# Performance work log

Hardware: AMD Instinct MI355X
Metric: run time of the kernel (lower is better)

## Reference

```python
import jax, jax.numpy as jnp
import numpy as np

B, T, E, D, A, H, C, K = 32, 1500, 512, 512, 512, 4, 10, 201
SHARPENING = 1.0


def setup_inputs() -> dict:
    key = jax.random.key(0)
    ks = jax.random.split(key, 11)
    def w(k, shape, fan_in):
        return jax.random.normal(k, shape, jnp.float32) / np.sqrt(fan_in).astype(np.float32)
    return {
        "enc_out": jax.random.normal(ks[0], (B, T, E), jnp.float32),
        "x_lens": jax.random.randint(ks[1], (B,), T // 2, T + 1),
        "dec_out": jax.random.normal(ks[2], (B, 1, D), jnp.float32),
        # previous-step attention weights: a valid distribution over T per head
        "aw_step": jax.nn.softmax(jax.random.normal(ks[3], (B, T, H), jnp.float32), axis=1),
        "w_enc": w(ks[4], (H, E, A), E),   # per-head LinearND(enc->att)
        "b_enc": jnp.zeros((H, A), jnp.float32),
        "w_dec": w(ks[5], (H, D, A), D),   # per-head LinearND(dec->att), no bias
        "w_conv": w(ks[6], (H, C, A), C),  # per-head LinearND(conv_ch->att), no bias
        "conv_k": w(ks[7], (H * C, 1, K), K),  # grouped 1D conv kernels (O,I,K), groups=H
        "v": w(ks[8], (H, A), A),          # per-head LinearND(att->1), no bias
        "w_mha": w(ks[9], (H * E, E), H * E),
        "b_mha": jnp.zeros((E,), jnp.float32),
    }


def reference(enc_out, x_lens, dec_out, aw_step, w_enc, b_enc, w_dec, w_conv, conv_k, v, w_mha, b_mha):
    b, t, e = enc_out.shape
    h = aw_step.shape[-1]
    c = w_conv.shape[1]
    k = conv_k.shape[-1]
    # enc_out_a: per-head encoder projection [B,T,H,A]
    enc_a = jnp.einsum('bte,hea->btha', enc_out, w_enc) + b_enc
    # decoder projection, broadcast over time [B,1,H,A]
    dec_a = jnp.einsum('bd,hda->bha', dec_out[:, 0], w_dec)[:, None]
    # location features: grouped 1D conv over previous attention weights
    aw_t = jnp.transpose(aw_step, (0, 2, 1))  # [B,H,T]
    conv = jax.lax.conv_general_dilated(
        aw_t, conv_k, window_strides=(1,), padding=[(k // 2, k // 2)],
        dimension_numbers=('NCH', 'OIH', 'NCH'), feature_group_count=h)  # [B,H*C,T]
    conv = conv.reshape(b, h, c, t).transpose(0, 3, 1, 2)  # [B,T,H,C]
    conv_a = jnp.einsum('bthc,hca->btha', conv, w_conv)
    # additive energy [B,T,H]
    energy = jnp.einsum('btha,ha->bth', jnp.tanh(enc_a + dec_a + conv_a), v)
    # original code multiplies energy by mask (1 valid, -1024 padded) then sharpening
    mask = jnp.where(jnp.arange(t)[None, :] < x_lens[:, None], 1.0, -1024.0).astype(energy.dtype)
    energy = energy * mask[:, :, None] * SHARPENING
    aw = jax.nn.softmax(energy, axis=1)  # softmax over time per head
    # per-head context, concatenated along feature dim -> [B,1,H*E]
    ctx = jnp.einsum('bte,bth->bhe', enc_out, aw).reshape(b, 1, h * e)
    ctx = ctx @ w_mha + b_mha  # [B,1,E]
    return ctx, aw
```

## Files before the change

kernel.cpp:

```cpp
#include <hip/hip_runtime.h>
#include <hip/hip_bf16.h>

#define BB 32
#define TT 1500
#define TP 1536
#define EE 512
#define HH 4
#define AA 512
#define NN 2048
#define CC 10
#define KCONV 201
#define KAUG 576

typedef __attribute__((ext_vector_type(8))) __bf16 bf16x8;
typedef __attribute__((ext_vector_type(4))) float f32x4;

__device__ __forceinline__ unsigned short f2bf(float x) {
    unsigned int u = __float_as_uint(x);
    u = (u + 0x7fffu + ((u >> 16) & 1u)) >> 16;
    return (unsigned short)u;
}
__device__ __forceinline__ float bf2f(unsigned short u) {
    return __uint_as_float(((unsigned int)u) << 16);
}
__device__ __forceinline__ void glds16(const void* g, void* l) {
    __builtin_amdgcn_global_load_lds(
        (const __attribute__((address_space(1))) unsigned int*)g,
        (__attribute__((address_space(3))) unsigned int*)l, 16, 0, 0);
}
__device__ __forceinline__ float tanh_fast(float x) {
    float e = __expf(x * 2.0f);
    return fmaf(-2.0f, __builtin_amdgcn_rcpf(e + 1.0f), 1.0f);
}

#define PREP_DEC0   0
#define PREP_CONV0  1024
#define PREP_WT0    8704
#define PREP_PAD0   13312
#define PREP_ENC0   20404
#define PREP_TOTAL  44404

__global__ __launch_bounds__(256) void k_prep(
    const float* __restrict__ enc, const int* __restrict__ xl,
    const float* __restrict__ dec_out, const float* __restrict__ aw_step,
    const float* __restrict__ w_enc, const float* __restrict__ b_enc,
    const float* __restrict__ w_dec, const float* __restrict__ w_conv,
    const float* __restrict__ conv_k,
    unsigned short* __restrict__ Whi, unsigned short* __restrict__ Wlo,
    unsigned short* __restrict__ Ahi, unsigned short* __restrict__ Alo,
    float* __restrict__ dec_a) {
    __shared__ float sbuf[456 + KCONV];
    const int bid = blockIdx.x;
    const int tid = threadIdx.x;

    if (bid < PREP_CONV0) {
        const int b  = bid >> 5;
        const int n0 = (bid & 31) * 64;
        const int n  = n0 + (tid & 63);
        const int dg = tid >> 6;
        const int h  = n >> 9, a = n & 511;
        const float* dp = dec_out + (size_t)b * 512 + dg * 128;
        const float* wp = w_dec + ((size_t)h * 512 + dg * 128) * 512 + a;
        float acc = 0.f;
#pragma unroll 8
        for (int d = 0; d < 128; ++d) acc += dp[d] * wp[(size_t)d * 512];
        sbuf[tid] = acc;
        __syncthreads();
        if (tid < 64) {
            float tot = sbuf[tid] + sbuf[tid + 64] + sbuf[tid + 128] + sbuf[tid + 192];
            dec_a[(size_t)b * NN + n0 + tid] = b_enc[n0 + tid] + tot;
        }
    } else if (bid < PREP_WT0) {
        int r = bid - PREP_CONV0;
        const int tch = r % 6;
        const int hc  = (r / 6) % 40;
        const int b   = r / 240;
        const int h   = hc / 10;
        const int t0  = tch * 256;
        float* sAw = sbuf;
        float* sK  = sbuf + 456;
        for (int i = tid; i < 456; i += 256) {
            int ts = t0 - 100 + i;
            sAw[i] = (ts >= 0 && ts < TT) ? aw_step[((size_t)b * TT + ts) * HH + h] : 0.f;
        }
        if (tid < KCONV) sK[tid] = conv_k[(size_t)hc * KCONV + tid];
        __syncthreads();
        int t = t0 + tid;
        if (t < TT) {
            float acc = 0.f;
            for (int k = 0; k < KCONV; ++k) acc += sAw[tid + k] * sK[k];
            size_t o = ((size_t)b * TP + t) * KAUG + 512 + hc;
            unsigned short hi = f2bf(acc);
            Ahi[o] = hi; Alo[o] = f2bf(acc - bf2f(hi));
        }
    } else if (bid < PREP_PAD0) {
        int idx = (bid - PREP_WT0) * 256 + tid;
        int n = idx / KAUG, k = idx % KAUG;
        int h = n >> 9, a = n & 511;
        float val = 0.f;
        if (k < 512) {
            val = w_enc[((size_t)h * 512 + k) * 512 + a];
        } else if (k < 552) {
            int j = k - 512; int h2 = j / 10, c = j % 10;
            if (h2 == h) val = w_conv[((size_t)h * 10 + c) * 512 + a];
        }
        unsigned short hi = f2bf(val);
        Whi[idx] = hi;
        Wlo[idx] = f2bf(val - bf2f(hi));
    } else if (bid < PREP_ENC0) {
        int idx = (bid - PREP_PAD0) * 256 + tid;
        const int tot1 = BB * 36 * KAUG;
        const int tot2 = BB * TT * 24;
        size_t o;
        if (idx < tot1) {
            int b = idx / (36 * KAUG); int r2 = idx % (36 * KAUG);
            int t = 1500 + r2 / KAUG;  int k = r2 % KAUG;
            o = ((size_t)b * TP + t) * KAUG + k;
        } else if (idx < tot1 + tot2) {
            int j = idx - tot1;
            int b = j / (TT * 24); int r2 = j % (TT * 24);
            int t = r2 / 24;       int k = 552 + r2 % 24;
            o = ((size_t)b * TP + t) * KAUG + k;
        } else return;
        Ahi[o] = 0; Alo[o] = 0;
    } else {
        long idx = (long)(bid - PREP_ENC0) * 256 + tid;
        if (idx >= 6144000L) return;
        long f = idx * 4;
        int b = (int)(f / 768000);
        int r2 = (int)(f % 768000);
        int t = r2 >> 9, e = r2 & 511;
        float4 vv = *reinterpret_cast<const float4*>(enc + f);
        ushort4 h4;
        h4.x = f2bf(vv.x); h4.y = f2bf(vv.y); h4.z = f2bf(vv.z); h4.w = f2bf(vv.w);
        size_t o = ((size_t)b * TP + t) * KAUG + e;
        *reinterpret_cast<ushort4*>(Ahi + o) = h4;
        if (((t & ~127) + 128) > xl[b]) {
            ushort4 l4;
            l4.x = f2bf(vv.x - bf2f(h4.x));
            l4.y = f2bf(vv.y - bf2f(h4.y));
            l4.z = f2bf(vv.z - bf2f(h4.z));
            l4.w = f2bf(vv.w - bf2f(h4.w));
            *reinterpret_cast<ushort4*>(Alo + o) = l4;
        }
    }
}

__global__ __launch_bounds__(256) void k_gemm(
    const unsigned short* __restrict__ Ahi, const unsigned short* __restrict__ Alo,
    const unsigned short* __restrict__ Whi, const unsigned short* __restrict__ Wlo,
    const float* __restrict__ dec_a, const float* __restrict__ vvec,
    const int* __restrict__ xl, float* __restrict__ energy) {
    __shared__ unsigned short lsAhi[128 * 32], lsAlo[128 * 32];
    __shared__ unsigned short lsBhi[128 * 32], lsBlo[128 * 32];
    const int ntile = blockIdx.x, mtile = blockIdx.y, b = blockIdx.z;
    const int tid = threadIdx.x;
    const int lane = tid & 63, wave = tid >> 6;
    const int wm = wave >> 1, wn = wave & 1;
    const int m0 = mtile * 128, n0 = ntile * 128;
    const int xlen = xl[b];

    f32x4 acc[4][4];
#pragma unroll
    for (int i = 0; i < 4; i++)
#pragma unroll
        for (int j = 0; j < 4; j++) acc[i][j] = (f32x4){0.f, 0.f, 0.f, 0.f};

    const int row = tid >> 2;
    const int ko  = (tid & 3) * 8;
    const size_t abase = ((size_t)b * TP + m0 + row) * KAUG + ko;
    const size_t bbase = ((size_t)n0 + row) * KAUG + ko;
    const int l1 = row * 32 + ko;
    const int l2 = l1 + 64 * 32;
    const int ar = wm * 64, br = wn * 64;
    const int fo = (lane & 15) * 32 + (lane >> 4) * 8;

    if (m0 + 128 > xlen) {
        for (int ks = 0; ks < 18; ++ks) {
            const int k0 = ks * 32;
            __syncthreads();
            glds16(Ahi + abase + k0,                     &lsAhi[l1]);
            glds16(Ahi + abase + k0 + (size_t)64 * KAUG, &lsAhi[l2]);
            glds16(Alo + abase + k0,                     &lsAlo[l1]);
            glds16(Alo + abase + k0 + (size_t)64 * KAUG, &lsAlo[l2]);
            glds16(Whi + bbase + k0,                     &lsBhi[l1]);
            glds16(Whi + bbase + k0 + (size_t)64 * KAUG, &lsBhi[l2]);
            glds16(Wlo + bbase + k0,                     &lsBlo[l1]);
            glds16(Wlo + bbase + k0 + (size_t)64 * KAUG, &lsBlo[l2]);
            asm volatile("s_waitcnt vmcnt(0)" ::: "memory");
            __syncthreads();

            bf16x8 ah[4], al[4], bh[4], bl[4];
#pragma unroll
            for (int i = 0; i < 4; i++) {
                ah[i] = *(const bf16x8*)&lsAhi[(ar + i * 16) * 32 + fo];
                al[i] = *(const bf16x8*)&lsAlo[(ar + i * 16) * 32 + fo];
                bh[i] = *(const bf16x8*)&lsBhi[(br + i * 16) * 32 + fo];
                bl[i] = *(const bf16x8*)&lsBlo[(br + i * 16) * 32 + fo];
            }
#pragma unroll
            for (int i = 0; i < 4; i++)
#pragma unroll
                for (int j = 0; j < 4; j++) {
                    acc[i][j] = __builtin_amdgcn_mfma_f32_16x16x32_bf16(ah[i], bh[j], acc[i][j], 0, 0, 0);
                    acc[i][j] = __builtin_amdgcn_mfma_f32_16x16x32_bf16(ah[i], bl[j], acc[i][j], 0, 0, 0);
                    acc[i][j] = __builtin_amdgcn_mfma_f32_16x16x32_bf16(al[i], bh[j], acc[i][j], 0, 0, 0);
                }
        }
    } else {
        for (int ks = 0; ks < 18; ++ks) {
            const int k0 = ks * 32;
            __syncthreads();
            glds16(Ahi + abase + k0,                     &lsAhi[l1]);
            glds16(Ahi + abase + k0 + (size_t)64 * KAUG, &lsAhi[l2]);
            glds16(Whi + bbase + k0,                     &lsBhi[l1]);
            glds16(Whi + bbase + k0 + (size_t)64 * KAUG, &lsBhi[l2]);
            asm volatile("s_waitcnt vmcnt(0)" ::: "memory");
            __syncthreads();

            bf16x8 ah[4], bh[4];
#pragma unroll
            for (int i = 0; i < 4; i++) {
                ah[i] = *(const bf16x8*)&lsAhi[(ar + i * 16) * 32 + fo];
                bh[i] = *(const bf16x8*)&lsBhi[(br + i * 16) * 32 + fo];
            }
#pragma unroll
            for (int i = 0; i < 4; i++)
#pragma unroll
                for (int j = 0; j < 4; j++)
                    acc[i][j] = __builtin_amdgcn_mfma_f32_16x16x32_bf16(ah[i], bh[j], acc[i][j], 0, 0, 0);
        }
    }

    const int h = ntile >> 2;
    const int kg = lane >> 4;
    float dv[4], vv[4];
#pragma unroll
    for (int j = 0; j < 4; j++) {
        int ng = n0 + wn * 64 + j * 16 + (lane & 15);
        dv[j] = dec_a[(size_t)b * NN + ng];
        vv[j] = vvec[ng];
    }
#pragma unroll
    for (int i = 0; i < 4; i++) {
        float part[4] = {0.f, 0.f, 0.f, 0.f};
#pragma unroll
        for (int j = 0; j < 4; j++)
#pragma unroll
            for (int r = 0; r < 4; r++)
                part[r] += tanh_fast(acc[i][j][r] + dv[j]) * vv[j];
#pragma unroll
        for (int r = 0; r < 4; r++) {
            float s = part[r];
            s += __shfl_xor(s, 1, 64);
            s += __shfl_xor(s, 2, 64);
            s += __shfl_xor(s, 4, 64);
            s += __shfl_xor(s, 8, 64);
            if ((lane & 15) == 0) {
                int t = m0 + wm * 64 + i * 16 + kg * 4 + r;
                if (t < TT)
                    atomicAdd(&energy[((size_t)b * HH + h) * TP + t], s);
            }
        }
    }
}

__global__ __launch_bounds__(512) void k_softmax(const float* __restrict__ energy,
                                                 const int* __restrict__ x_lens,
                                                 float* __restrict__ aw) {
    const int b = blockIdx.x >> 2, h = blockIdx.x & 3;
    const int tid = threadIdx.x;
    __shared__ float sE[TT];
    __shared__ float red[512];
    const int xlen = x_lens[b];
    float lmax = -3.4e38f;
    for (int t = tid; t < TT; t += 512) {
        float e = energy[((size_t)b * HH + h) * TP + t];
        float m = (t < xlen) ? e : e * -1024.0f;
        sE[t] = m;
        lmax = fmaxf(lmax, m);
    }
    red[tid] = lmax; __syncthreads();
    for (int s = 256; s > 0; s >>= 1) { if (tid < s) red[tid] = fmaxf(red[tid], red[tid + s]); __syncthreads(); }
    float mx = red[0]; __syncthreads();
    float lsum = 0.f;
    for (int t = tid; t < TT; t += 512) {
        float ex = expf(sE[t] - mx);
        sE[t] = ex; lsum += ex;
    }
    red[tid] = lsum; __syncthreads();
    for (int s = 256; s > 0; s >>= 1) { if (tid < s) red[tid] += red[tid + s]; __syncthreads(); }
    float sum = red[0];
    for (int t = tid; t < TT; t += 512)
        aw[((size_t)b * TT + t) * HH + h] = sE[t] / sum;
}

__global__ __launch_bounds__(512) void k_ctx(const float* __restrict__ enc,
                                             const float* __restrict__ aw,
                                             float* __restrict__ ctx_h) {
    const int chunk = blockIdx.x, b = blockIdx.y;
    const int t0 = chunk * 128;
    const int nt = (TT - t0 < 128) ? (TT - t0) : 128;
    __shared__ float sA[128 * 4];
    const int tid = threadIdx.x;
    for (int i = tid; i < nt * 4; i += 512)
        sA[i] = aw[((size_t)b * TT + t0) * HH + i];
    __syncthreads();
    float a0 = 0.f, a1 = 0.f, a2 = 0.f, a3 = 0.f;
    const float* ep = enc + ((size_t)b * TT + t0) * EE + tid;
    if (nt == 128) {
#pragma unroll 8
        for (int tt = 0; tt < 128; ++tt) {
            float ev = ep[(size_t)tt * EE];
            a0 += sA[tt * 4 + 0] * ev; a1 += sA[tt * 4 + 1] * ev;
            a2 += sA[tt * 4 + 2] * ev; a3 += sA[tt * 4 + 3] * ev;
        }
    } else {
        for (int tt = 0; tt < nt; ++tt) {
            float ev = ep[(size_t)tt * EE];
            a0 += sA[tt * 4 + 0] * ev; a1 += sA[tt * 4 + 1] * ev;
            a2 += sA[tt * 4 + 2] * ev; a3 += sA[tt * 4 + 3] * ev;
        }
    }
    atomicAdd(&ctx_h[((size_t)b * HH + 0) * EE + tid], a0);
    atomicAdd(&ctx_h[((size_t)b * HH + 1) * EE + tid], a1);
    atomicAdd(&ctx_h[((size_t)b * HH + 2) * EE + tid], a2);
    atomicAdd(&ctx_h[((size_t)b * HH + 3) * EE + tid], a3);
}

__global__ __launch_bounds__(256) void k_mha(const float* __restrict__ ctx_h,
                                             const float* __restrict__ w_mha,
                                             const float* __restrict__ b_mha,
                                             float* __restrict__ out) {
    __shared__ float sred[256];
    const int tid = threadIdx.x;
    const int b  = blockIdx.x >> 2;
    const int eo = ((blockIdx.x & 3) << 7) + (tid & 127);
    const int kg = tid >> 7;
    const float* c = ctx_h + (size_t)b * NN + kg * 1024;
    const float* w = w_mha + ((size_t)kg * 1024) * EE + eo;
    float acc = 0.f;
#pragma unroll 8
    for (int k = 0; k < 1024; ++k) acc += c[k] * w[(size_t)k * EE];
    sred[tid] = acc;
    __syncthreads();
    if (tid < 128)
        out[(size_t)b * EE + eo] = b_mha[eo] + sred[tid] + sred[tid + 128];
}

extern "C" void kernel_launch(void* const* d_in, const int* in_sizes, int n_in,
                              void* d_out, int out_size, void* d_ws, size_t ws_size,
                              hipStream_t stream) {
    (void)in_sizes; (void)n_in; (void)out_size;
    const float* enc    = (const float*)d_in[0];
    const int*   xlen   = (const int*)d_in[1];
    const float* dec    = (const float*)d_in[2];
    const float* aw_in  = (const float*)d_in[3];
    const float* w_enc  = (const float*)d_in[4];
    const float* b_enc  = (const float*)d_in[5];
    const float* w_dec  = (const float*)d_in[6];
    const float* w_conv = (const float*)d_in[7];
    const float* convk  = (const float*)d_in[8];
    const float* v      = (const float*)d_in[9];
    const float* w_mha  = (const float*)d_in[10];
    const float* b_mha  = (const float*)d_in[11];
    float* out = (float*)d_out;

    char* ws = (char*)d_ws;
    unsigned short* Whi = (unsigned short*)ws;
    unsigned short* Wlo = Whi + (size_t)NN * KAUG;
    unsigned short* Ahi = (unsigned short*)(ws + 4718592);
    unsigned short* Alo = Ahi + (size_t)BB * TP * KAUG;
    float* dec_a  = (float*)(ws + 117964800);
    float* energy = (float*)(ws + 118226944);
    float* ctx_h  = (float*)(ws + 119013376);
    (void)ws_size;

    hipMemsetAsync(energy, 0, 786432 + 262144, stream);

    k_prep<<<dim3(PREP_TOTAL), 256, 0, stream>>>(enc, xlen, dec, aw_in, w_enc, b_enc,
                                                 w_dec, w_conv, convk,
                                                 Whi, Wlo, Ahi, Alo, dec_a);
    k_gemm<<<dim3(16, 12, BB), 256, 0, stream>>>(Ahi, Alo, Whi, Wlo, dec_a, v, xlen, energy);
    k_softmax<<<dim3(BB * HH), 512, 0, stream>>>(energy, xlen, out + 16384);
    k_ctx <<<dim3(12, BB), 512, 0, stream>>>(enc, out + 16384, ctx_h);
    k_mha <<<dim3(128), 256, 0, stream>>>(ctx_h, w_mha, b_mha, out);
}
```

Before: 597.1 us.

## Fuse enc bf16 split into GEMM, transpose weights via LDS, trim softmax/ctx

The GEMM now reads fp32 encoder rows straight from global memory and converts them to bf16 hi/lo in registers before storing to LDS. This drops the large prep pass that materialised a padded bf16 copy of enc_out. Conv features go to a small separate buffer, the weight transpose goes through a padded LDS tile, and GEMM blocks are remapped so neighbouring tiles land on the same XCD. Softmax moves to 1024 threads with fast exp and a reciprocal, and ctx blocks skip chunks whose weights are all zero. The trade-off is register-path conversion and a software-prefetched A load instead of async global-to-LDS copies.

```diff
diff --git a/kernel.cpp b/kernel.cpp
--- a/kernel.cpp
+++ b/kernel.cpp
@@ -32,24 +32,31 @@
     float e = __expf(x * 2.0f);
     return fmaf(-2.0f, __builtin_amdgcn_rcpf(e + 1.0f), 1.0f);
 }
+__device__ __forceinline__ unsigned int pkbf(float x, float y) {
+    float2 f{x, y};
+    __hip_bfloat162 h2 = __float22bfloat162_rn(f);
+    return *reinterpret_cast<unsigned int*>(&h2);
+}
+__device__ __forceinline__ void split2(float x, float y, unsigned int& h, unsigned int& l) {
+    unsigned short hx = f2bf(x), hy = f2bf(y);
+    h = ((unsigned int)hy << 16) | hx;
+    l = pkbf(x - bf2f(hx), y - bf2f(hy));
+}
 
 #define PREP_DEC0   0
 #define PREP_CONV0  1024
 #define PREP_WT0    8704
-#define PREP_PAD0   13312
-#define PREP_ENC0   20404
-#define PREP_TOTAL  44404
+#define PREP_TOTAL  8992
 
 __global__ __launch_bounds__(256) void k_prep(
-    const float* __restrict__ enc, const int* __restrict__ xl,
     const float* __restrict__ dec_out, const float* __restrict__ aw_step,
     const float* __restrict__ w_enc, const float* __restrict__ b_enc,
     const float* __restrict__ w_dec, const float* __restrict__ w_conv,
     const float* __restrict__ conv_k,
     unsigned short* __restrict__ Whi, unsigned short* __restrict__ Wlo,
-    unsigned short* __restrict__ Ahi, unsigned short* __restrict__ Alo,
+    unsigned short* __restrict__ Chi, unsigned short* __restrict__ Clo,
     float* __restrict__ dec_a) {
-    __shared__ float sbuf[456 + KCONV];
+    __shared__ float sh[64 * 65];
     const int bid = blockIdx.x;
     const int tid = threadIdx.x;
 
@@ -64,10 +71,10 @@
         float acc = 0.f;
 #pragma unroll 8
         for (int d = 0; d < 128; ++d) acc += dp[d] * wp[(size_t)d * 512];
-        sbuf[tid] = acc;
+        sh[tid] = acc;
         __syncthreads();
         if (tid < 64) {
-            float tot = sbuf[tid] + sbuf[tid + 64] + sbuf[tid + 128] + sbuf[tid + 192];
+            float tot = sh[tid] + sh[tid + 64] + sh[tid + 128] + sh[tid + 192];
             dec_a[(size_t)b * NN + n0 + tid] = b_enc[n0 + tid] + tot;
         }
     } else if (bid < PREP_WT0) {
@@ -77,83 +84,77 @@
         const int b   = r / 240;
         const int h   = hc / 10;
         const int t0  = tch * 256;
-        float* sAw = sbuf;
-        float* sK  = sbuf + 456;
+        float* sAw = sh;
         for (int i = tid; i < 456; i += 256) {
             int ts = t0 - 100 + i;
             sAw[i] = (ts >= 0 && ts < TT) ? aw_step[((size_t)b * TT + ts) * HH + h] : 0.f;
         }
-        if (tid < KCONV) sK[tid] = conv_k[(size_t)hc * KCONV + tid];
         __syncthreads();
         int t = t0 + tid;
         if (t < TT) {
+            const float* ck = conv_k + (size_t)hc * KCONV;
             float acc = 0.f;
-            for (int k = 0; k < KCONV; ++k) acc += sAw[tid + k] * sK[k];
-            size_t o = ((size_t)b * TP + t) * KAUG + 512 + hc;
+#pragma unroll 4
+            for (int k = 0; k < KCONV; ++k) acc += sAw[tid + k] * ck[k];
+            size_t o = ((size_t)b * TP + t) * 64 + hc;
             unsigned short hi = f2bf(acc);
-            Ahi[o] = hi; Alo[o] = f2bf(acc - bf2f(hi));
-        }
-    } else if (bid < PREP_PAD0) {
-        int idx = (bid - PREP_WT0) * 256 + tid;
-        int n = idx / KAUG, k = idx % KAUG;
-        int h = n >> 9, a = n & 511;
-        float val = 0.f;
-        if (k < 512) {
-            val = w_enc[((size_t)h * 512 + k) * 512 + a];
-        } else if (k < 552) {
-            int j = k - 512; int h2 = j / 10, c = j % 10;
-            if (h2 == h) val = w_conv[((size_t)h * 10 + c) * 512 + a];
-        }
-        unsigned short hi = f2bf(val);
-        Whi[idx] = hi;
-        Wlo[idx] = f2bf(val - bf2f(hi));
-    } else if (bid < PREP_ENC0) {
-        int idx = (bid - PREP_PAD0) * 256 + tid;
-        const int tot1 = BB * 36 * KAUG;
-        const int tot2 = BB * TT * 24;
-        size_t o;
-        if (idx < tot1) {
-            int b = idx / (36 * KAUG); int r2 = idx % (36 * KAUG);
-            int t = 1500 + r2 / KAUG;  int k = r2 % KAUG;
-            o = ((size_t)b * TP + t) * KAUG + k;
-        } else if (idx < tot1 + tot2) {
-            int j = idx - tot1;
-            int b = j / (TT * 24); int r2 = j % (TT * 24);
-            int t = r2 / 24;       int k = 552 + r2 % 24;
-            o = ((size_t)b * TP + t) * KAUG + k;
-        } else return;
-        Ahi[o] = 0; Alo[o] = 0;
+            Chi[o] = hi; Clo[o] = f2bf(acc - bf2f(hi));
+        }
     } else {
-        long idx = (long)(bid - PREP_ENC0) * 256 + tid;
-        if (idx >= 6144000L) return;
-        long f = idx * 4;
-        int b = (int)(f / 768000);
-        int r2 = (int)(f % 768000);
-        int t = r2 >> 9, e = r2 & 511;
-        float4 vv = *reinterpret_cast<const float4*>(enc + f);
-        ushort4 h4;
-        h4.x = f2bf(vv.x); h4.y = f2bf(vv.y); h4.z = f2bf(vv.z); h4.w = f2bf(vv.w);
-        size_t o = ((size_t)b * TP + t) * KAUG + e;
-        *reinterpret_cast<ushort4*>(Ahi + o) = h4;
-        if (((t & ~127) + 128) > xl[b]) {
-            ushort4 l4;
-            l4.x = f2bf(vv.x - bf2f(h4.x));
-            l4.y = f2bf(vv.y - bf2f(h4.y));
-            l4.z = f2bf(vv.z - bf2f(h4.z));
-            l4.w = f2bf(vv.w - bf2f(h4.w));
-            *reinterpret_cast<ushort4*>(Alo + o) = l4;
+        int r = bid - PREP_WT0;
+        const int h  = r / 72;
+        const int rr = r % 72;
+        const int at = rr / 9;
+        const int kt = rr % 9;
+        const int a0 = at * 64;
+        if (kt < 8) {
+            const int k0 = kt * 64;
+#pragma unroll
+            for (int it = 0; it < 16; ++it) {
+                int kk = it * 4 + (tid >> 6);
+                int aa = tid & 63;
+                sh[kk * 65 + aa] = w_enc[((size_t)h * 512 + k0 + kk) * 512 + a0 + aa];
+            }
+            __syncthreads();
+#pragma unroll
+            for (int it = 0; it < 16; ++it) {
+                int nl = it * 4 + (tid >> 6);
+                int kk = tid & 63;
+                float val = sh[kk * 65 + nl];
+                size_t o = ((size_t)h * 512 + a0 + nl) * KAUG + k0 + kk;
+                unsigned short hi = f2bf(val);
+                Whi[o] = hi; Wlo[o] = f2bf(val - bf2f(hi));
+            }
+        } else {
+#pragma unroll
+            for (int it = 0; it < 16; ++it) {
+                int nl = it * 4 + (tid >> 6);
+                int j  = tid & 63;
+                float val = 0.f;
+                if (j < 40 && (j / 10) == h)
+                    val = w_conv[((size_t)h * 10 + (j % 10)) * 512 + a0 + nl];
+                size_t o = ((size_t)h * 512 + a0 + nl) * KAUG + 512 + j;
+                unsigned short hi = f2bf(val);
+                Whi[o] = hi; Wlo[o] = f2bf(val - bf2f(hi));
+            }
         }
     }
 }
 
 __global__ __launch_bounds__(256) void k_gemm(
-    const unsigned short* __restrict__ Ahi, const unsigned short* __restrict__ Alo,
+    const float* __restrict__ enc,
+    const unsigned short* __restrict__ Chi, const unsigned short* __restrict__ Clo,
     const unsigned short* __restrict__ Whi, const unsigned short* __restrict__ Wlo,
     const float* __restrict__ dec_a, const float* __restrict__ vvec,
     const int* __restrict__ xl, float* __restrict__ energy) {
-    __shared__ unsigned short lsAhi[128 * 32], lsAlo[128 * 32];
-    __shared__ unsigned short lsBhi[128 * 32], lsBlo[128 * 32];
-    const int ntile = blockIdx.x, mtile = blockIdx.y, b = blockIdx.z;
+    __shared__ unsigned short lsAhi[4096], lsAlo[4096];
+    __shared__ unsigned short lsBhi[4096], lsBlo[4096];
+    const int id = blockIdx.x;
+    const int xcd = id & 7;
+    const int wq  = id >> 3;
+    const int ntile = wq & 15;
+    const int mb = xcd * 48 + (wq >> 4);
+    const int b = mb & 31, mtile = mb >> 5;
     const int tid = threadIdx.x;
     const int lane = tid & 63, wave = tid >> 6;
     const int wm = wave >> 1, wn = wave & 1;
@@ -168,25 +169,97 @@
 
     const int row = tid >> 2;
     const int ko  = (tid & 3) * 8;
-    const size_t abase = ((size_t)b * TP + m0 + row) * KAUG + ko;
     const size_t bbase = ((size_t)n0 + row) * KAUG + ko;
-    const int l1 = row * 32 + ko;
-    const int l2 = l1 + 64 * 32;
+    const size_t cbase = ((size_t)b * TP + m0 + row) * 64 + ko;
+    const int l1 = tid * 8;
+    const int l2 = l1 + 2048;
     const int ar = wm * 64, br = wn * 64;
     const int fo = (lane & 15) * 32 + (lane >> 4) * 8;
 
-    if (m0 + 128 > xlen) {
+    const float* ap0 = enc + ((size_t)b * TT + m0 + row) * 512 + ko;
+    const float* ap1 = ap0 + (size_t)64 * 512;
+
+    if (m0 + 128 <= xlen) {
+        float4 fa0 = *(const float4*)(ap0);
+        float4 fa1 = *(const float4*)(ap0 + 4);
+        float4 fa2 = *(const float4*)(ap1);
+        float4 fa3 = *(const float4*)(ap1 + 4);
         for (int ks = 0; ks < 18; ++ks) {
             const int k0 = ks * 32;
             __syncthreads();
-            glds16(Ahi + abase + k0,                     &lsAhi[l1]);
-            glds16(Ahi + abase + k0 + (size_t)64 * KAUG, &lsAhi[l2]);
-            glds16(Alo + abase + k0,                     &lsAlo[l1]);
-            glds16(Alo + abase + k0 + (size_t)64 * KAUG, &lsAlo[l2]);
+            glds16(Whi + bbase + k0,                     &lsBhi[l1]);
+            glds16(Whi + bbase + k0 + (size_t)64 * KAUG, &lsBhi[l2]);
+            if (ks < 16) {
+                uint4 w0, w1;
+                w0.x = pkbf(fa0.x, fa0.y); w0.y = pkbf(fa0.z, fa0.w);
+                w0.z = pkbf(fa1.x, fa1.y); w0.w = pkbf(fa1.z, fa1.w);
+                w1.x = pkbf(fa2.x, fa2.y); w1.y = pkbf(fa2.z, fa2.w);
+                w1.z = pkbf(fa3.x, fa3.y); w1.w = pkbf(fa3.z, fa3.w);
+                *reinterpret_cast<uint4*>(&lsAhi[l1]) = w0;
+                *reinterpret_cast<uint4*>(&lsAhi[l2]) = w1;
+                if (ks < 15) {
+                    const int nk = k0 + 32;
+                    fa0 = *(const float4*)(ap0 + nk);
+                    fa1 = *(const float4*)(ap0 + nk + 4);
+                    fa2 = *(const float4*)(ap1 + nk);
+                    fa3 = *(const float4*)(ap1 + nk + 4);
+                }
+            } else {
+                glds16(Chi + cbase + (ks - 16) * 32,        &lsAhi[l1]);
+                glds16(Chi + cbase + (ks - 16) * 32 + 4096, &lsAhi[l2]);
+            }
+            asm volatile("s_waitcnt vmcnt(0)" ::: "memory");
+            __syncthreads();
+
+            bf16x8 ah[4], bh[4];
+#pragma unroll
+            for (int i = 0; i < 4; i++) {
+                ah[i] = *(const bf16x8*)&lsAhi[(ar + i * 16) * 32 + fo];
+                bh[i] = *(const bf16x8*)&lsBhi[(br + i * 16) * 32 + fo];
+            }
+#pragma unroll
+            for (int i = 0; i < 4; i++)
+#pragma unroll
+                for (int j = 0; j < 4; j++)
+                    acc[i][j] = __builtin_amdgcn_mfma_f32_16x16x32_bf16(ah[i], bh[j], acc[i][j], 0, 0, 0);
+        }
+    } else {
+        const bool g1 = (m0 + row + 64) < TT;
+        const float4 z4 = {0.f, 0.f, 0.f, 0.f};
+        float4 fa0 = *(const float4*)(ap0);
+        float4 fa1 = *(const float4*)(ap0 + 4);
+        float4 fa2 = g1 ? *(const float4*)(ap1) : z4;
+        float4 fa3 = g1 ? *(const float4*)(ap1 + 4) : z4;
+        for (int ks = 0; ks < 18; ++ks) {
+            const int k0 = ks * 32;
+            __syncthreads();
             glds16(Whi + bbase + k0,                     &lsBhi[l1]);
             glds16(Whi + bbase + k0 + (size_t)64 * KAUG, &lsBhi[l2]);
             glds16(Wlo + bbase + k0,                     &lsBlo[l1]);
             glds16(Wlo + bbase + k0 + (size_t)64 * KAUG, &lsBlo[l2]);
+            if (ks < 16) {
+                uint4 h0, h1, e0, e1;
+                split2(fa0.x, fa0.y, h0.x, e0.x); split2(fa0.z, fa0.w, h0.y, e0.y);
+                split2(fa1.x, fa1.y, h0.z, e0.z); split2(fa1.z, fa1.w, h0.w, e0.w);
+                split2(fa2.x, fa2.y, h1.x, e1.x); split2(fa2.z, fa2.w, h1.y, e1.y);
+                split2(fa3.x, fa3.y, h1.z, e1.z); split2(fa3.z, fa3.w, h1.w, e1.w);
+                *reinterpret_cast<uint4*>(&lsAhi[l1]) = h0;
+                *reinterpret_cast<uint4*>(&lsAhi[l2]) = h1;
+                *reinterpret_cast<uint4*>(&lsAlo[l1]) = e0;
+                *reinterpret_cast<uint4*>(&lsAlo[l2]) = e1;
+                if (ks < 15) {
+                    const int nk = k0 + 32;
+                    fa0 = *(const float4*)(ap0 + nk);
+                    fa1 = *(const float4*)(ap0 + nk + 4);
+                    fa2 = g1 ? *(const float4*)(ap1 + nk) : z4;
+                    fa3 = g1 ? *(const float4*)(ap1 + nk + 4) : z4;
+                }
+            } else {
+                glds16(Chi + cbase + (ks - 16) * 32,        &lsAhi[l1]);
+                glds16(Chi + cbase + (ks - 16) * 32 + 4096, &lsAhi[l2]);
+                glds16(Clo + cbase + (ks - 16) * 32,        &lsAlo[l1]);
+                glds16(Clo + cbase + (ks - 16) * 32 + 4096, &lsAlo[l2]);
+            }
             asm volatile("s_waitcnt vmcnt(0)" ::: "memory");
             __syncthreads();
 
@@ -206,29 +279,6 @@
                     acc[i][j] = __builtin_amdgcn_mfma_f32_16x16x32_bf16(ah[i], bl[j], acc[i][j], 0, 0, 0);
                     acc[i][j] = __builtin_amdgcn_mfma_f32_16x16x32_bf16(al[i], bh[j], acc[i][j], 0, 0, 0);
                 }
-        }
-    } else {
-        for (int ks = 0; ks < 18; ++ks) {
-            const int k0 = ks * 32;
-            __syncthreads();
-            glds16(Ahi + abase + k0,                     &lsAhi[l1]);
-            glds16(Ahi + abase + k0 + (size_t)64 * KAUG, &lsAhi[l2]);
-            glds16(Whi + bbase + k0,                     &lsBhi[l1]);
-            glds16(Whi + bbase + k0 + (size_t)64 * KAUG, &lsBhi[l2]);
-            asm volatile("s_waitcnt vmcnt(0)" ::: "memory");
-            __syncthreads();
-
-            bf16x8 ah[4], bh[4];
-#pragma unroll
-            for (int i = 0; i < 4; i++) {
-                ah[i] = *(const bf16x8*)&lsAhi[(ar + i * 16) * 32 + fo];
-                bh[i] = *(const bf16x8*)&lsBhi[(br + i * 16) * 32 + fo];
-            }
-#pragma unroll
-            for (int i = 0; i < 4; i++)
-#pragma unroll
-                for (int j = 0; j < 4; j++)
-                    acc[i][j] = __builtin_amdgcn_mfma_f32_16x16x32_bf16(ah[i], bh[j], acc[i][j], 0, 0, 0);
         }
     }
 
@@ -265,34 +315,34 @@
     }
 }
 
-__global__ __launch_bounds__(512) void k_softmax(const float* __restrict__ energy,
-                                                 const int* __restrict__ x_lens,
-                                                 float* __restrict__ aw) {
+__global__ __launch_bounds__(1024) void k_softmax(const float* __restrict__ energy,
+                                                  const int* __restrict__ x_lens,
+                                                  float* __restrict__ aw) {
     const int b = blockIdx.x >> 2, h = blockIdx.x & 3;
     const int tid = threadIdx.x;
     __shared__ float sE[TT];
-    __shared__ float red[512];
+    __shared__ float red[1024];
     const int xlen = x_lens[b];
     float lmax = -3.4e38f;
-    for (int t = tid; t < TT; t += 512) {
+    for (int t = tid; t < TT; t += 1024) {
         float e = energy[((size_t)b * HH + h) * TP + t];
         float m = (t < xlen) ? e : e * -1024.0f;
         sE[t] = m;
         lmax = fmaxf(lmax, m);
     }
     red[tid] = lmax; __syncthreads();
-    for (int s = 256; s > 0; s >>= 1) { if (tid < s) red[tid] = fmaxf(red[tid], red[tid + s]); __syncthreads(); }
+    for (int s = 512; s > 0; s >>= 1) { if (tid < s) red[tid] = fmaxf(red[tid], red[tid + s]); __syncthreads(); }
     float mx = red[0]; __syncthreads();
     float lsum = 0.f;
-    for (int t = tid; t < TT; t += 512) {
-        float ex = expf(sE[t] - mx);
+    for (int t = tid; t < TT; t += 1024) {
+        float ex = __expf(sE[t] - mx);
         sE[t] = ex; lsum += ex;
     }
     red[tid] = lsum; __syncthreads();
-    for (int s = 256; s > 0; s >>= 1) { if (tid < s) red[tid] += red[tid + s]; __syncthreads(); }
-    float sum = red[0];
-    for (int t = tid; t < TT; t += 512)
-        aw[((size_t)b * TT + t) * HH + h] = sE[t] / sum;
+    for (int s = 512; s > 0; s >>= 1) { if (tid < s) red[tid] += red[tid + s]; __syncthreads(); }
+    float rs = 1.0f / red[0];
+    for (int t = tid; t < TT; t += 1024)
+        aw[((size_t)b * TT + t) * HH + h] = sE[t] * rs;
 }
 
 __global__ __launch_bounds__(512) void k_ctx(const float* __restrict__ enc,
@@ -302,10 +352,17 @@
     const int t0 = chunk * 128;
     const int nt = (TT - t0 < 128) ? (TT - t0) : 128;
     __shared__ float sA[128 * 4];
+    __shared__ int s_nz;
     const int tid = threadIdx.x;
-    for (int i = tid; i < nt * 4; i += 512)
-        sA[i] = aw[((size_t)b * TT + t0) * HH + i];
+    if (tid == 0) s_nz = 0;
     __syncthreads();
+    for (int i = tid; i < nt * 4; i += 512) {
+        float w = aw[((size_t)b * TT + t0) * HH + i];
+        sA[i] = w;
+        if (w != 0.f) s_nz = 1;
+    }
+    __syncthreads();
+    if (!s_nz) return;
     float a0 = 0.f, a1 = 0.f, a2 = 0.f, a3 = 0.f;
     const float* ep = enc + ((size_t)b * TT + t0) * EE + tid;
     if (nt == 128) {
@@ -368,21 +425,21 @@
 
     char* ws = (char*)d_ws;
     unsigned short* Whi = (unsigned short*)ws;
-    unsigned short* Wlo = Whi + (size_t)NN * KAUG;
-    unsigned short* Ahi = (unsigned short*)(ws + 4718592);
-    unsigned short* Alo = Ahi + (size_t)BB * TP * KAUG;
-    float* dec_a  = (float*)(ws + 117964800);
-    float* energy = (float*)(ws + 118226944);
-    float* ctx_h  = (float*)(ws + 119013376);
+    unsigned short* Wlo = (unsigned short*)(ws + 2359296);
+    unsigned short* Chi = (unsigned short*)(ws + 4718592);
+    unsigned short* Clo = (unsigned short*)(ws + 11010048);
+    float* dec_a  = (float*)(ws + 17301504);
+    float* energy = (float*)(ws + 17563648);
+    float* ctx_h  = (float*)(ws + 18350080);
     (void)ws_size;
 
     hipMemsetAsync(energy, 0, 786432 + 262144, stream);
 
-    k_prep<<<dim3(PREP_TOTAL), 256, 0, stream>>>(enc, xlen, dec, aw_in, w_enc, b_enc,
+    k_prep<<<dim3(PREP_TOTAL), 256, 0, stream>>>(dec, aw_in, w_enc, b_enc,
                                                  w_dec, w_conv, convk,
-                                                 Whi, Wlo, Ahi, Alo, dec_a);
-    k_gemm<<<dim3(16, 12, BB), 256, 0, stream>>>(Ahi, Alo, Whi, Wlo, dec_a, v, xlen, energy);
-    k_softmax<<<dim3(BB * HH), 512, 0, stream>>>(energy, xlen, out + 16384);
+                                                 Whi, Wlo, Chi, Clo, dec_a);
+    k_gemm<<<dim3(6144), 256, 0, stream>>>(enc, Chi, Clo, Whi, Wlo, dec_a, v, xlen, energy);
+    k_softmax<<<dim3(BB * HH), 1024, 0, stream>>>(energy, xlen, out + 16384);
     k_ctx <<<dim3(12, BB), 512, 0, stream>>>(enc, out + 16384, ctx_h);
     k_mha <<<dim3(128), 256, 0, stream>>>(ctx_h, w_mha, b_mha, out);
 }
```

New measurement: 790.1 us. +32.3%, slower.
